# Kernel tuning notes

Hardware: AMD Instinct MI355X
Metric: run time of the kernel (lower is better)

The kernel has to match this reference:

```python
import jax, jax.numpy as jnp
import numpy as np

N_NODES = 50000
N_EDGES = 300000
D = 256
N_RELS = 500


def setup_inputs() -> dict:
    key = jax.random.key(0)
    ks = jax.random.split(key, 12)
    s = 1.0 / np.sqrt(D)  # keep activations O(1) through the dense transforms
    return {
        "h": jax.random.normal(ks[0], (N_NODES, D), dtype=jnp.float32),
        "prev_h": jax.random.normal(ks[1], (N_NODES, D), dtype=jnp.float32),
        "emb_rel": jax.random.normal(ks[2], (N_RELS, D), dtype=jnp.float32),
        "norm": jax.random.uniform(ks[3], (N_NODES, 1), dtype=jnp.float32),
        "weight_neighbor": jax.random.normal(ks[4], (D, D), dtype=jnp.float32) * s,
        "loop_weight": jax.random.normal(ks[5], (D, D), dtype=jnp.float32) * s,
        "evolve_loop_weight": jax.random.normal(ks[6], (D, D), dtype=jnp.float32) * s,
        "skip_connect_weight": jax.random.normal(ks[7], (D, D), dtype=jnp.float32) * s,
        "skip_connect_bias": jnp.zeros((D,), dtype=jnp.float32),
        "src": jax.random.randint(ks[8], (N_EDGES,), 0, N_NODES),
        "dst": jax.random.randint(ks[9], (N_EDGES,), 0, N_NODES),
        "etype": jax.random.randint(ks[10], (N_EDGES,), 0, N_RELS),
    }


def reference(h, prev_h, emb_rel, norm, weight_neighbor, loop_weight,
              evolve_loop_weight, skip_connect_weight, skip_connect_bias,
              src, dst, etype):
    n_nodes = h.shape[0]
    # msg_func: per-edge gather of src features + relation embedding, dense transform
    msg = (h[src] + emb_rel[etype]) @ weight_neighbor          # [E, D]
    # fn.sum: segment-sum messages into destination nodes
    agg = jax.ops.segment_sum(msg, dst, num_segments=n_nodes)  # [N, D]
    # apply_func: multiply by per-node norm
    agg = agg * norm
    # self-loop: loop_weight where in_degree > 0, evolve_loop_weight otherwise
    in_deg = jax.ops.segment_sum(jnp.ones_like(dst), dst, num_segments=n_nodes)
    has_in = (in_deg > 0)[:, None]
    loop_message = jnp.where(has_in, h @ loop_weight, h @ evolve_loop_weight)
    # skip connection gate
    skip_weight = jax.nn.sigmoid(prev_h @ skip_connect_weight + skip_connect_bias)
    node_repr = skip_weight * (agg + loop_message) + (1.0 - skip_weight) * prev_h
    return jax.nn.relu(node_repr)
```

## Files before the change

### kernel.cpp

```cpp
#include <hip/hip_runtime.h>
#include <hip/hip_bf16.h>
#include <cstdint>
#include <cstddef>

#define N_NODES 50000
#define N_EDGES 300000
#define DIM     256
#define KTOT    768
#define N_RELS  500

#define SCAN_BLK  256
#define SCAN_NBLK ((N_NODES + SCAN_BLK - 1) / SCAN_BLK)

typedef unsigned short u16;
typedef __attribute__((ext_vector_type(8))) short short8v;
typedef __attribute__((ext_vector_type(4))) float float4v;

static __device__ __forceinline__ u16 f2bf(float f) {
    union { float f; unsigned u; } v; v.f = f;
    unsigned u = v.u;
    unsigned r = u + 0x7FFFu + ((u >> 16) & 1u);
    return (u16)(r >> 16);
}

__global__ void wt_kernel(const float* __restrict__ Wn, const float* __restrict__ Wl,
                          const float* __restrict__ Wsc, u16* __restrict__ Wt) {
    int k = blockIdx.x;
    int d = threadIdx.x;
    const float* W = (k < 256) ? Wn : ((k < 512) ? Wl : Wsc);
    int kk = k & 255;
    Wt[(size_t)d * KTOT + k] = f2bf(W[kk * DIM + d]);
}

__global__ void hist_kernel(const int* __restrict__ dstv, int* __restrict__ deg) {
    int e = blockIdx.x * 256 + threadIdx.x;
    if (e < N_EDGES) atomicAdd(&deg[dstv[e]], 1);
}

__global__ void scanA_kernel(const int* __restrict__ deg, int* __restrict__ excl_local,
                             int* __restrict__ block_sum) {
    __shared__ int sdata[SCAN_BLK];
    int t = threadIdx.x, i = blockIdx.x * SCAN_BLK + t;
    int v = (i < N_NODES) ? deg[i] : 0;
    sdata[t] = v;
    __syncthreads();
    for (int off = 1; off < SCAN_BLK; off <<= 1) {
        int u = (t >= off) ? sdata[t - off] : 0;
        __syncthreads();
        sdata[t] += u;
        __syncthreads();
    }
    if (i < N_NODES) excl_local[i] = sdata[t] - v;
    if (t == SCAN_BLK - 1) block_sum[blockIdx.x] = sdata[t];
}

__global__ void scanB_kernel(const int* __restrict__ block_sum, int* __restrict__ block_base,
                             int* __restrict__ offsets) {
    __shared__ int sdata[SCAN_NBLK];
    int t = threadIdx.x;
    int v = (t < SCAN_NBLK) ? block_sum[t] : 0;
    if (t < SCAN_NBLK) sdata[t] = v;
    __syncthreads();
    for (int off = 1; off < SCAN_NBLK; off <<= 1) {
        int u = (t >= off && t < SCAN_NBLK) ? sdata[t - off] : 0;
        __syncthreads();
        if (t < SCAN_NBLK) sdata[t] += u;
        __syncthreads();
    }
    if (t < SCAN_NBLK) block_base[t] = sdata[t] - v;
    if (t == SCAN_NBLK - 1) offsets[N_NODES] = sdata[t];
}

__global__ void scanC_kernel(const int* __restrict__ excl_local, const int* __restrict__ block_base,
                             int* __restrict__ offsets, int* __restrict__ cursor) {
    int i = blockIdx.x * SCAN_BLK + threadIdx.x;
    if (i < N_NODES) {
        int e = block_base[blockIdx.x] + excl_local[i];
        offsets[i] = e; cursor[i] = e;
    }
}

__global__ void scatter_kernel(const int* __restrict__ src, const int* __restrict__ dstv,
                               const int* __restrict__ et, int* __restrict__ cursor,
                               unsigned* __restrict__ esee) {
    int e = blockIdx.x * 256 + threadIdx.x;
    if (e >= N_EDGES) return;
    int d = dstv[e];
    int pos = atomicAdd(&cursor[d], 1);
    esee[pos] = (unsigned)src[e] * N_RELS + (unsigned)et[e];
}

__global__ void agg_kernel(const float* __restrict__ h, const float* __restrict__ emb,
                           const float* __restrict__ norm, const int* __restrict__ offsets,
                           const unsigned* __restrict__ esee,
                           u16* __restrict__ Xa, int* __restrict__ wl_count, int* __restrict__ wl) {
    int wave = (blockIdx.x * 256 + threadIdx.x) >> 6;
    int lane = threadIdx.x & 63;
    if (wave >= N_NODES) return;
    int n = wave;
    int s0 = offsets[n], s1 = offsets[n + 1];
    int c4 = lane * 4;
    float4 acc = make_float4(0.f, 0.f, 0.f, 0.f);
    for (int e = s0; e < s1; e++) {
        unsigned v = esee[e];
        unsigned s = v / N_RELS;
        unsigned t = v - s * N_RELS;
        float4 hv = *(const float4*)(h   + (size_t)s * DIM + c4);
        float4 ev = *(const float4*)(emb + (size_t)t * DIM + c4);
        acc.x += hv.x + ev.x; acc.y += hv.y + ev.y;
        acc.z += hv.z + ev.z; acc.w += hv.w + ev.w;
    }
    float nr = norm[n];
    u16 o[4] = { f2bf(acc.x * nr), f2bf(acc.y * nr), f2bf(acc.z * nr), f2bf(acc.w * nr) };
    *(ushort4*)(Xa + (size_t)n * DIM + c4) = *(const ushort4*)o;
    if (lane == 0 && s1 == s0) { int idx = atomicAdd(wl_count, 1); wl[idx] = n; }
}

#define LDSP 72
__launch_bounds__(512, 4)
__global__ void gemm_kernel(const u16* __restrict__ Xa, const u16* __restrict__ Wt,
                            const float* __restrict__ h, const float* __restrict__ prev_h,
                            const float* __restrict__ bias, float* __restrict__ out) {
    __shared__ u16 Xs[128 * LDSP];
    __shared__ u16 Ws[256 * LDSP];
    int tid = threadIdx.x;
    int wave = tid >> 6, lane = tid & 63, q = lane >> 4, m16 = lane & 15;
    int wm = (wave >> 2) * 64;
    int wn = (wave & 3) * 64;
    int m0 = blockIdx.x * 128;

    float4v acc1[4][4], acc2[4][4];
#pragma unroll
    for (int i = 0; i < 4; i++)
#pragma unroll
        for (int j = 0; j < 4; j++) { acc1[i][j] = (float4v)0.f; acc2[i][j] = (float4v)0.f; }

    int bxr = tid >> 3, bxc = (tid & 7) * 8;
    int fxr = tid >> 4, fxc = (tid & 15) * 4;
    int wd  = tid >> 3, wp  = (tid & 7) * 8;

    for (int kt = 0; kt < 12; kt++) {
        int koff = (kt & 3) * 64;
        if (kt < 4) {
#pragma unroll
            for (int r = 0; r < 2; r++) {
                int row = bxr + r * 64;
                int grow = min(m0 + row, N_NODES - 1);
                *(uint4*)(&Xs[row * LDSP + bxc]) =
                    *(const uint4*)(Xa + (size_t)grow * DIM + koff + bxc);
            }
        } else {
            const float* F = (kt < 8) ? h : prev_h;
#pragma unroll
            for (int r = 0; r < 4; r++) {
                int row = fxr + r * 32;
                int grow = min(m0 + row, N_NODES - 1);
                float4 fv = *(const float4*)(F + (size_t)grow * DIM + koff + fxc);
                u16 o[4] = { f2bf(fv.x), f2bf(fv.y), f2bf(fv.z), f2bf(fv.w) };
                *(ushort4*)(&Xs[row * LDSP + fxc]) = *(const ushort4*)o;
            }
        }
#pragma unroll
        for (int it = 0; it < 4; it++) {
            int d = wd + it * 64;
            *(uint4*)(&Ws[d * LDSP + wp]) =
                *(const uint4*)(Wt + (size_t)d * KTOT + kt * 64 + wp);
        }
        __syncthreads();
#pragma unroll
        for (int kk = 0; kk < 2; kk++) {
            short8v af[4], bfr[4];
#pragma unroll
            for (int mi = 0; mi < 4; mi++)
                af[mi] = *(const short8v*)(&Xs[(wm + mi * 16 + m16) * LDSP + kk * 32 + q * 8]);
#pragma unroll
            for (int ni = 0; ni < 4; ni++)
                bfr[ni] = *(const short8v*)(&Ws[(wn + ni * 16 + m16) * LDSP + kk * 32 + q * 8]);
            if (kt < 8) {
#pragma unroll
                for (int mi = 0; mi < 4; mi++)
#pragma unroll
                    for (int ni = 0; ni < 4; ni++)
                        acc1[mi][ni] = __builtin_amdgcn_mfma_f32_16x16x32_bf16(
                            af[mi], bfr[ni], acc1[mi][ni], 0, 0, 0);
            } else {
#pragma unroll
                for (int mi = 0; mi < 4; mi++)
#pragma unroll
                    for (int ni = 0; ni < 4; ni++)
                        acc2[mi][ni] = __builtin_amdgcn_mfma_f32_16x16x32_bf16(
                            af[mi], bfr[ni], acc2[mi][ni], 0, 0, 0);
            }
        }
        __syncthreads();
    }

#pragma unroll
    for (int mi = 0; mi < 4; mi++) {
#pragma unroll
        for (int ni = 0; ni < 4; ni++) {
            int d = wn + ni * 16 + m16;
            float b = bias[d];
#pragma unroll
            for (int r = 0; r < 4; r++) {
                int node = m0 + wm + mi * 16 + q * 4 + r;
                if (node < N_NODES) {
                    float S  = acc2[mi][ni][r] + b;
                    float sw = 1.f / (1.f + __expf(-S));
                    float ph = prev_h[(size_t)node * DIM + d];
                    float v  = sw * acc1[mi][ni][r] + (1.f - sw) * ph;
                    out[(size_t)node * DIM + d] = fmaxf(v, 0.f);
                }
            }
        }
    }
}

__global__ void fixup_kernel(const float* __restrict__ h, const float* __restrict__ prev_h,
                             const float* __restrict__ We, const float* __restrict__ Wsc,
                             const float* __restrict__ bias, const int* __restrict__ wl_count,
                             const int* __restrict__ wl, float* __restrict__ out) {
    __shared__ float ph[DIM], hh[DIM];
    int d = threadIdx.x;
    int cnt = *wl_count;
    for (int i = blockIdx.x; i < cnt; i += gridDim.x) {
        int n = wl[i];
        ph[d] = prev_h[(size_t)n * DIM + d];
        hh[d] = h[(size_t)n * DIM + d];
        __syncthreads();
        float s = 0.f, l = 0.f;
        for (int k = 0; k < DIM; k++) {
            s += ph[k] * Wsc[k * DIM + d];
            l += hh[k] * We[k * DIM + d];
        }
        float sw = 1.f / (1.f + __expf(-(s + bias[d])));
        float v = sw * l + (1.f - sw) * ph[d];
        out[(size_t)n * DIM + d] = fmaxf(v, 0.f);
        __syncthreads();
    }
}

extern "C" void kernel_launch(void* const* d_in, const int* in_sizes, int n_in,
                              void* d_out, int out_size, void* d_ws, size_t ws_size,
                              hipStream_t stream) {
    const float* h      = (const float*)d_in[0];
    const float* prev_h = (const float*)d_in[1];
    const float* emb    = (const float*)d_in[2];
    const float* norm   = (const float*)d_in[3];
    const float* Wn     = (const float*)d_in[4];
    const float* Wl     = (const float*)d_in[5];
    const float* We     = (const float*)d_in[6];
    const float* Wsc    = (const float*)d_in[7];
    const float* bias   = (const float*)d_in[8];
    const int*   src    = (const int*)d_in[9];
    const int*   dstv   = (const int*)d_in[10];
    const int*   et     = (const int*)d_in[11];
    float* out = (float*)d_out;

    char* ws = (char*)d_ws;
    size_t off = 0;
    auto alloc = [&](size_t bytes) -> char* {
        char* p = ws + off; off += (bytes + 255) & ~(size_t)255; return p;
    };
    u16* Xa      = (u16*)alloc((size_t)N_NODES * DIM * 2);
    u16* Wt      = (u16*)alloc((size_t)DIM * KTOT * 2);
    int* deg     = (int*)alloc((size_t)N_NODES * 4);
    int* wlcnt   = (int*)alloc(16);
    int* wl      = (int*)alloc((size_t)N_NODES * 4);
    int* offsets = (int*)alloc((size_t)(N_NODES + 1) * 4);
    int* cursor  = (int*)alloc((size_t)N_NODES * 4);
    unsigned* esee = (unsigned*)alloc((size_t)N_EDGES * 4);
    int* excl    = (int*)alloc((size_t)N_NODES * 4);
    int* bsum    = (int*)alloc((size_t)SCAN_NBLK * 4);
    int* bbase   = (int*)alloc((size_t)SCAN_NBLK * 4);

    hipMemsetAsync(deg, 0, (size_t)N_NODES * 4, stream);
    hipMemsetAsync(wlcnt, 0, 4, stream);

    wt_kernel<<<KTOT, 256, 0, stream>>>(Wn, Wl, Wsc, Wt);
    hist_kernel<<<(N_EDGES + 255) / 256, 256, 0, stream>>>(dstv, deg);
    scanA_kernel<<<SCAN_NBLK, SCAN_BLK, 0, stream>>>(deg, excl, bsum);
    scanB_kernel<<<1, SCAN_BLK, 0, stream>>>(bsum, bbase, offsets);
    scanC_kernel<<<SCAN_NBLK, SCAN_BLK, 0, stream>>>(excl, bbase, offsets, cursor);
    scatter_kernel<<<(N_EDGES + 255) / 256, 256, 0, stream>>>(src, dstv, et, cursor, esee);
    agg_kernel<<<(N_NODES + 3) / 4, 256, 0, stream>>>(h, emb, norm, offsets, esee, Xa, wlcnt, wl);
    gemm_kernel<<<(N_NODES + 127) / 128, 512, 0, stream>>>(Xa, Wt, h, prev_h, bias, out);
    fixup_kernel<<<256, 256, 0, stream>>>(h, prev_h, We, Wsc, bias, wlcnt, wl, out);
}
```

Baseline: 367.9 us.

## Prefetch next GEMM K-tile into registers and shrink block to 64 rows

The GEMM kernel now uses 64-row tiles with 256 threads (4 waves each covering 64 output columns) instead of 128-row tiles with 512 threads. It also register-prefetches the next K-tile of activations and weights from global memory while the current tile's MFMAs run, so load latency overlaps compute. In exchange, weight tiles are reloaded twice as often per node and register pressure rises from the prefetch buffers.

```diff
diff --git a/kernel.cpp b/kernel.cpp
--- a/kernel.cpp
+++ b/kernel.cpp
@@ -117,17 +117,16 @@
 }
 
 #define LDSP 72
-__launch_bounds__(512, 4)
+__launch_bounds__(256, 2)
 __global__ void gemm_kernel(const u16* __restrict__ Xa, const u16* __restrict__ Wt,
                             const float* __restrict__ h, const float* __restrict__ prev_h,
                             const float* __restrict__ bias, float* __restrict__ out) {
-    __shared__ u16 Xs[128 * LDSP];
+    __shared__ u16 Xs[64 * LDSP];
     __shared__ u16 Ws[256 * LDSP];
     int tid = threadIdx.x;
     int wave = tid >> 6, lane = tid & 63, q = lane >> 4, m16 = lane & 15;
-    int wm = (wave >> 2) * 64;
-    int wn = (wave & 3) * 64;
-    int m0 = blockIdx.x * 128;
+    int wn = wave * 64;
+    int m0 = blockIdx.x * 64;
 
     float4v acc1[4][4], acc2[4][4];
 #pragma unroll
@@ -135,44 +134,67 @@
 #pragma unroll
         for (int j = 0; j < 4; j++) { acc1[i][j] = (float4v)0.f; acc2[i][j] = (float4v)0.f; }
 
-    int bxr = tid >> 3, bxc = (tid & 7) * 8;
-    int fxr = tid >> 4, fxc = (tid & 15) * 4;
-    int wd  = tid >> 3, wp  = (tid & 7) * 8;
+    int xrow = tid >> 2, xcol = (tid & 3) * 16;
+    int wp   = tid & 7,  wd   = tid >> 3;
+    int grow = min(m0 + xrow, N_NODES - 1);
+
+    uint4  xreg[2];
+    float4 freg[4];
+    uint4  wreg[8];
+
+    {
+        const u16* p = Xa + (size_t)grow * DIM + xcol;
+        xreg[0] = *(const uint4*)p;
+        xreg[1] = *(const uint4*)(p + 8);
+#pragma unroll
+        for (int it = 0; it < 8; it++)
+            wreg[it] = *(const uint4*)(Wt + (size_t)(wd + it * 32) * KTOT + wp * 8);
+    }
 
     for (int kt = 0; kt < 12; kt++) {
-        int koff = (kt & 3) * 64;
         if (kt < 4) {
-#pragma unroll
-            for (int r = 0; r < 2; r++) {
-                int row = bxr + r * 64;
-                int grow = min(m0 + row, N_NODES - 1);
-                *(uint4*)(&Xs[row * LDSP + bxc]) =
-                    *(const uint4*)(Xa + (size_t)grow * DIM + koff + bxc);
+            *(uint4*)(&Xs[xrow * LDSP + xcol])     = xreg[0];
+            *(uint4*)(&Xs[xrow * LDSP + xcol + 8]) = xreg[1];
+        } else {
+            u16 o[16];
+#pragma unroll
+            for (int j = 0; j < 4; j++) {
+                o[j*4+0] = f2bf(freg[j].x); o[j*4+1] = f2bf(freg[j].y);
+                o[j*4+2] = f2bf(freg[j].z); o[j*4+3] = f2bf(freg[j].w);
             }
-        } else {
-            const float* F = (kt < 8) ? h : prev_h;
-#pragma unroll
-            for (int r = 0; r < 4; r++) {
-                int row = fxr + r * 32;
-                int grow = min(m0 + row, N_NODES - 1);
-                float4 fv = *(const float4*)(F + (size_t)grow * DIM + koff + fxc);
-                u16 o[4] = { f2bf(fv.x), f2bf(fv.y), f2bf(fv.z), f2bf(fv.w) };
-                *(ushort4*)(&Xs[row * LDSP + fxc]) = *(const ushort4*)o;
+            *(uint4*)(&Xs[xrow * LDSP + xcol])     = ((const uint4*)o)[0];
+            *(uint4*)(&Xs[xrow * LDSP + xcol + 8]) = ((const uint4*)o)[1];
+        }
+#pragma unroll
+        for (int it = 0; it < 8; it++)
+            *(uint4*)(&Ws[(wd + it * 32) * LDSP + wp * 8]) = wreg[it];
+        __syncthreads();
+
+        if (kt < 11) {
+            int nk = kt + 1;
+            int koff = (nk & 3) * 64;
+            if (nk < 4) {
+                const u16* p = Xa + (size_t)grow * DIM + koff + xcol;
+                xreg[0] = *(const uint4*)p;
+                xreg[1] = *(const uint4*)(p + 8);
+            } else {
+                const float* F = (nk < 8) ? h : prev_h;
+                const float* p = F + (size_t)grow * DIM + koff + xcol;
+#pragma unroll
+                for (int j = 0; j < 4; j++)
+                    freg[j] = *(const float4*)(p + j * 4);
             }
-        }
-#pragma unroll
-        for (int it = 0; it < 4; it++) {
-            int d = wd + it * 64;
-            *(uint4*)(&Ws[d * LDSP + wp]) =
-                *(const uint4*)(Wt + (size_t)d * KTOT + kt * 64 + wp);
-        }
-        __syncthreads();
+#pragma unroll
+            for (int it = 0; it < 8; it++)
+                wreg[it] = *(const uint4*)(Wt + (size_t)(wd + it * 32) * KTOT + nk * 64 + wp * 8);
+        }
+
 #pragma unroll
         for (int kk = 0; kk < 2; kk++) {
             short8v af[4], bfr[4];
 #pragma unroll
             for (int mi = 0; mi < 4; mi++)
-                af[mi] = *(const short8v*)(&Xs[(wm + mi * 16 + m16) * LDSP + kk * 32 + q * 8]);
+                af[mi] = *(const short8v*)(&Xs[(mi * 16 + m16) * LDSP + kk * 32 + q * 8]);
 #pragma unroll
             for (int ni = 0; ni < 4; ni++)
                 bfr[ni] = *(const short8v*)(&Ws[(wn + ni * 16 + m16) * LDSP + kk * 32 + q * 8]);
@@ -203,7 +225,7 @@
             float b = bias[d];
 #pragma unroll
             for (int r = 0; r < 4; r++) {
-                int node = m0 + wm + mi * 16 + q * 4 + r;
+                int node = m0 + mi * 16 + q * 4 + r;
                 if (node < N_NODES) {
                     float S  = acc2[mi][ni][r] + b;
                     float sw = 1.f / (1.f + __expf(-S));
@@ -284,6 +306,6 @@
     scanC_kernel<<<SCAN_NBLK, SCAN_BLK, 0, stream>>>(excl, bbase, offsets, cursor);
     scatter_kernel<<<(N_EDGES + 255) / 256, 256, 0, stream>>>(src, dstv, et, cursor, esee);
     agg_kernel<<<(N_NODES + 3) / 4, 256, 0, stream>>>(h, emb, norm, offsets, esee, Xa, wlcnt, wl);
-    gemm_kernel<<<(N_NODES + 127) / 128, 512, 0, stream>>>(Xa, Wt, h, prev_h, bias, out);
+    gemm_kernel<<<(N_NODES + 63) / 64, 256, 0, stream>>>(Xa, Wt, h, prev_h, bias, out);
     fixup_kernel<<<256, 256, 0, stream>>>(h, prev_h, We, Wsc, bias, wlcnt, wl, out);
 }
```

New measurement: 466.6 us. 26.8% more time.
